# Performance work log

Hardware: AMD Instinct MI355X
Metric: run time of the kernel (lower is better)

The kernel has to match this reference:

```python
import jax, jax.numpy as jnp
import numpy as np

B, T, D_MODEL, N_HEADS = 2, 2048, 1024, 16
HEAD_DIM = D_MODEL // N_HEADS          # 64
CODE_SIZE = HEAD_DIM // 4              # 16


def setup_inputs() -> dict:
    key = jax.random.key(0)
    k1, k2, k3, k4 = jax.random.split(key, 4)
    x = jax.random.normal(k1, (B, T, D_MODEL), dtype=jnp.float32)
    # nn.Linear weights (out_features, in_features), fan-in init scale
    w_qkv = jax.random.normal(k2, (3 * D_MODEL, D_MODEL), dtype=jnp.float32) / np.sqrt(D_MODEL)
    w_out = jax.random.normal(k3, (D_MODEL, D_MODEL), dtype=jnp.float32) / np.sqrt(D_MODEL)
    fc_code = jax.random.normal(k4, (1, N_HEADS, CODE_SIZE, HEAD_DIM), dtype=jnp.float32)
    return {"x": x, "w_qkv": w_qkv, "w_out": w_out, "fc_code": fc_code}


def reference(x, w_qkv, w_out, fc_code):
    Bx, Tx, _ = x.shape
    scale = HEAD_DIM ** (-0.5)
    qkv = x @ w_qkv.T                                   # (B,T,3*d_model)
    # split_heads with Hs=head_dim on 3*d_model -> (B, 3*nH, T, Hs), then chunk on head axis
    qkv = qkv.reshape(Bx, Tx, 3 * N_HEADS, HEAD_DIM).transpose(0, 2, 1, 3)
    q, k, v = qkv[:, :N_HEADS], qkv[:, N_HEADS:2 * N_HEADS], qkv[:, 2 * N_HEADS:]
    code = fc_code[0]                                   # (nH, C, Hs)
    q = jnp.einsum('bhtd,hcd->bhtc', q, code) * scale   # (B,H,T,C)
    k = jnp.einsum('bhtd,hcd->bhtc', k, code) * scale
    q = jax.nn.softmax(q, axis=-1) * scale
    # causal branch (mask is None)
    k_exp = jnp.exp(k - jnp.max(k, axis=2, keepdims=True))       # (B,H,T,C)
    k_exp_cumsum = jnp.cumsum(k_exp, axis=2)                      # (B,H,T,C)
    kv_cumsum = jnp.cumsum(jnp.einsum('bhtc,bhtd->bhtcd', k_exp, v), axis=2)  # (B,H,T,C,D)
    kv = kv_cumsum / (k_exp_cumsum[..., None] + 1e-9)
    xo = jnp.einsum('bhtc,bhtcd->bhtd', q, kv)                    # (B,H,T,D)
    xo = xo.transpose(0, 2, 1, 3).reshape(Bx, Tx, D_MODEL)        # cat_heads
    return xo @ w_out.T
```

## Files before the change

### kernel.cpp

```cpp
#include <hip/hip_runtime.h>
#include <math.h>

#define B_    2
#define T_    2048
#define D_    1024
#define H_    16
#define HD_   64
#define C_    16
#define SCALE_ 0.125f
#define L_    128
#define NC_   16
#define QKP_  512

typedef __attribute__((ext_vector_type(8))) short short8;
typedef __attribute__((ext_vector_type(4))) float f32x4;

__device__ inline float b2f(uint32_t u16) {
    return __uint_as_float(u16 << 16);
}
__device__ inline ushort f2b(float f) {
    uint32_t u = __float_as_uint(f);
    return (ushort)((u + 0x7FFFu + ((u >> 16) & 1u)) >> 16);
}
__device__ inline uint32_t pack2(float a, float b) {
    return (uint32_t)f2b(a) | ((uint32_t)f2b(b) << 16);
}
__device__ inline void unpack2(uint32_t w, float& a, float& b) {
    a = b2f(w & 0xffffu); b = __uint_as_float(w & 0xffff0000u);
}
__device__ inline void unpack8(uint4 raw, float* dst) {
    unpack2(raw.x, dst[0], dst[1]);
    unpack2(raw.y, dst[2], dst[3]);
    unpack2(raw.z, dst[4], dst[5]);
    unpack2(raw.w, dst[6], dst[7]);
}
__device__ __forceinline__ void gll16(const ushort* g, ushort* l) {
    __builtin_amdgcn_global_load_lds(
        (const __attribute__((address_space(1))) void*)g,
        (__attribute__((address_space(3))) void*)l, 16, 0, 0);
}

__global__ __launch_bounds__(256)
void prep_inputs_kernel(const float* __restrict__ x, const float* __restrict__ w_qkv,
                        const float* __restrict__ w_out, const float* __restrict__ code,
                        ushort* __restrict__ xb, ushort* __restrict__ WallB,
                        ushort* __restrict__ WoB) {
    const int bid = blockIdx.x;
    if (bid < 3072) {
        const float* in;
        ushort* out;
        int i;
        if (bid < 2048) {
            in = x; out = xb;
            i = bid * 2048 + threadIdx.x * 8;
        } else {
            const int sub = bid - 2048;
            const int isW = sub >> 9;
            in = isW ? w_out : (w_qkv + (size_t)2048 * 1024);
            out = isW ? WoB : (WallB + (size_t)512 * 1024);
            i = (sub & 511) * 2048 + threadIdx.x * 8;
        }
        float4 a = *(const float4*)(in + i);
        float4 b = *(const float4*)(in + i + 4);
        uint4 o;
        o.x = pack2(a.x, a.y); o.y = pack2(a.z, a.w);
        o.z = pack2(b.x, b.y); o.w = pack2(b.z, b.w);
        *(uint4*)(out + i) = o;
    } else {
        const int sub = bid - 3072;
        const int isK = sub >> 8;
        const int row = sub & 255;
        const int h = row >> 4;
        __shared__ float cs[HD_];
        if (threadIdx.x < HD_) cs[threadIdx.x] = code[row * HD_ + threadIdx.x];
        __syncthreads();
        const float* wbase = w_qkv + (size_t)(isK * D_ + h * HD_) * D_;
        ushort* outp = WallB + (size_t)(isK * 256 + row) * D_;
        for (int e = threadIdx.x; e < D_; e += 256) {
            float acc = 0.f;
            #pragma unroll 8
            for (int d = 0; d < HD_; ++d) acc += wbase[(size_t)d * D_ + e] * cs[d];
            outp[e] = f2b(acc * SCALE_);
        }
    }
}

template<int MODE>
__global__ __launch_bounds__(256)
void gemm_bf16_kernel(const ushort* __restrict__ A, const ushort* __restrict__ Bw,
                      void* __restrict__ Cv, ushort* __restrict__ vTout,
                      int M, int N, int K) {
    __shared__ ushort As[2][128 * 64];
    __shared__ ushort Bs[2][64 * 64];
    const int tid  = threadIdx.x;
    const int wave = tid >> 6;
    const int lane = tid & 63;

    const int gx = gridDim.x;
    int f = blockIdx.y * gx + blockIdx.x;
    const int nwg = gx * gridDim.y;
    if ((nwg & 7) == 0) f = (f & 7) * (nwg >> 3) + (f >> 3);
    const int row0 = (f / gx) * 128;
    const int col0 = (f % gx) * 64;

    f32x4 acc[2][4];
    #pragma unroll
    for (int m = 0; m < 2; ++m)
        #pragma unroll
        for (int n = 0; n < 4; ++n) acc[m][n] = (f32x4){0.f, 0.f, 0.f, 0.f};

    const int srow = lane >> 3;
    const int kA   = ((lane & 7) ^ srow) << 3;
    const int lane15 = lane & 15;
    const int lhi    = lane >> 4;
    const int axor   = (lane15 & 7) << 4;

    const int NT = K >> 6;

    auto STAGE = [&](int buf, int kk) {
        #pragma unroll
        for (int i = 0; i < 6; ++i) {
            const int sg = wave * 6 + i;
            if (sg < 16) {
                const int r = sg * 8 + srow;
                gll16(A + (size_t)(row0 + r) * K + kk + kA, &As[buf][sg * 512]);
            } else {
                const int sb = sg - 16;
                const int r = sb * 8 + srow;
                gll16(Bw + (size_t)(col0 + r) * K + kk + kA, &Bs[buf][sb * 512]);
            }
        }
    };

    STAGE(0, 0);
    __syncthreads();

    for (int it = 0; it < NT; ++it) {
        const int cur = it & 1;
        if (it + 1 < NT) STAGE(cur ^ 1, (it + 1) << 6);
        const char* Ab = (const char*)As[cur];
        const char* Bb = (const char*)Bs[cur];
        #pragma unroll
        for (int s = 0; s < 2; ++s) {
            short8 af[2], bf[4];
            #pragma unroll
            for (int m = 0; m < 2; ++m) {
                const int r = wave * 32 + m * 16 + lane15;
                const int off = (r * 128 + s * 64 + lhi * 16) ^ axor;
                af[m] = *(const short8*)(Ab + off);
            }
            #pragma unroll
            for (int n = 0; n < 4; ++n) {
                const int r = n * 16 + lane15;
                const int off = (r * 128 + s * 64 + lhi * 16) ^ axor;
                bf[n] = *(const short8*)(Bb + off);
            }
            #pragma unroll
            for (int m = 0; m < 2; ++m)
                #pragma unroll
                for (int n = 0; n < 4; ++n)
                    acc[m][n] = __builtin_amdgcn_mfma_f32_16x16x32_bf16(
                        af[m], bf[n], acc[m][n], 0, 0, 0);
        }
        __syncthreads();
    }

    #pragma unroll
    for (int m = 0; m < 2; ++m) {
        #pragma unroll
        for (int n = 0; n < 4; ++n) {
            const int row = row0 + wave * 32 + m * 16 + lhi * 4;
            const int col = col0 + n * 16 + lane15;
            if (MODE == 0) {
                float* C = (float*)Cv;
                #pragma unroll
                for (int j = 0; j < 4; ++j)
                    C[(size_t)(row + j) * N + col] = acc[m][n][j];
            } else if (MODE == 1) {
                ushort* C = (ushort*)Cv;
                #pragma unroll
                for (int j = 0; j < 4; ++j)
                    C[(size_t)(row + j) * N + col] = f2b(acc[m][n][j]);
            } else {
                if (col0 < 512) {
                    ushort* C = (ushort*)Cv;
                    #pragma unroll
                    for (int j = 0; j < 4; ++j)
                        C[(size_t)(row + j) * QKP_ + col] = f2b(acc[m][n][j]);
                } else {
                    const int dg = col - 512;
                    const int h = dg >> 6, d = dg & 63;
                    const int b = row >> 11;
                    const int t = row & 2047;
                    ushort* p = vTout + ((size_t)((b * 16 + h) * 64 + d)) * 2048 + t;
                    *(uint2*)p = make_uint2(pack2(acc[m][n][0], acc[m][n][1]),
                                            pack2(acc[m][n][2], acc[m][n][3]));
                }
            }
        }
    }
}

__global__ __launch_bounds__(256)
void prep_attn_kernel(const ushort* __restrict__ qkcv, const ushort* __restrict__ vT,
                      float* __restrict__ ke_loc, float* __restrict__ kv_loc) {
    const int bid = blockIdx.x;
    const int chunk = bid & (NC_ - 1);
    const int bh = bid >> 4;
    const int b = bh >> 4, h = bh & 15;
    const int t0 = chunk * L_;
    const int tid = threadIdx.x;
    __shared__ float ke_s[L_][C_];
    __shared__ float gsum[C_][16];

    {
        const int t = tid >> 1, c0 = (tid & 1) * 8;
        uint4 raw = *(const uint4*)(qkcv + (size_t)(b * T_ + t0 + t) * QKP_ + 256 + h * C_ + c0);
        float f[8]; unpack8(raw, f);
        #pragma unroll
        for (int j = 0; j < 8; ++j) ke_s[t][c0 + j] = __expf(f[j]);
    }
    __syncthreads();

    const int d = tid & 63;
    const int cw = tid >> 6;
    const ushort* vrow = vT + ((size_t)(bh * 64 + d)) * 2048 + t0;
    float a0 = 0.f, a1 = 0.f, a2 = 0.f, a3 = 0.f;
    for (int kb = 0; kb < 16; ++kb) {
        uint4 raw = *(const uint4*)(vrow + kb * 8);
        float v8[8]; unpack8(raw, v8);
        #pragma unroll
        for (int u = 0; u < 8; ++u) {
            const int t = kb * 8 + u;
            a0 += ke_s[t][cw * 4 + 0] * v8[u];
            a1 += ke_s[t][cw * 4 + 1] * v8[u];
            a2 += ke_s[t][cw * 4 + 2] * v8[u];
            a3 += ke_s[t][cw * 4 + 3] * v8[u];
        }
    }
    float* kvb = kv_loc + (size_t)bid * 1024 + d;
    kvb[(cw * 4 + 0) * 64] = a0;
    kvb[(cw * 4 + 1) * 64] = a1;
    kvb[(cw * 4 + 2) * 64] = a2;
    kvb[(cw * 4 + 3) * 64] = a3;

    {
        const int cc = tid & 15, g = tid >> 4;
        float s = 0.f;
        #pragma unroll
        for (int u = 0; u < 8; ++u) s += ke_s[g * 8 + u][cc];
        gsum[cc][g] = s;
    }
    __syncthreads();
    if (tid < C_) {
        float s = 0.f;
        #pragma unroll
        for (int g = 0; g < 16; ++g) s += gsum[tid][g];
        ke_loc[(size_t)bid * C_ + tid] = s;
    }
}

__global__ __launch_bounds__(256)
void intra_kernel(const ushort* __restrict__ qkcv, const ushort* __restrict__ vT,
                  const float* __restrict__ ke_loc, const float* __restrict__ kv_loc,
                  ushort* __restrict__ xob) {
    const int bid = blockIdx.x;
    const int chunk = bid & (NC_ - 1);
    const int bh = bid >> 4;
    const int b = bh >> 4, h = bh & 15;
    const int t0 = chunk * L_;
    const int tid = threadIdx.x;
    const int wave = tid >> 6, lane = tid & 63;
    const int l15 = lane & 15, lhi = lane >> 4;

    __shared__ __align__(16) ushort ke_bf[128 * 32];
    __shared__ __align__(16) ushort qn_bf[128 * 32];
    __shared__ __align__(16) ushort Vt_s[64 * 128];
    __shared__ __align__(16) ushort Pl[128 * 128];
    __shared__ __align__(16) ushort S0t[64 * 32];
    __shared__ float kesum_s[128][16];
    __shared__ float gsum[16][16];
    __shared__ float e0s[16];

    char* keB = (char*)ke_bf;
    char* qnB = (char*)qn_bf;
    char* vtB = (char*)Vt_s;
    char* plB = (char*)Pl;
    char* s0B = (char*)S0t;

    {
        const int t = tid >> 1, c0 = (tid & 1) * 8;
        uint4 raw = *(const uint4*)(qkcv + (size_t)(b * T_ + t0 + t) * QKP_ + 256 + h * C_ + c0);
        float f[8]; unpack8(raw, f);
        uint4 o;
        o.x = pack2(__expf(f[0]), __expf(f[1]));
        o.y = pack2(__expf(f[2]), __expf(f[3]));
        o.z = pack2(__expf(f[4]), __expf(f[5]));
        o.w = pack2(__expf(f[6]), __expf(f[7]));
        const int swz = ((t >> 1) & 3) << 4;
        *(uint4*)(keB + ((t * 64 + c0 * 2) ^ swz)) = o;
        *(uint4*)(keB + ((t * 64 + 32 + c0 * 2) ^ swz)) = make_uint4(0, 0, 0, 0);
    }
    {
        const int d = tid >> 2, q = tid & 3;
        const ushort* src = vT + ((size_t)bh * 64 + d) * 2048 + t0 + q * 32;
        const int swz = (d & 15) << 4;
        #pragma unroll
        for (int i = 0; i < 4; ++i) {
            uint4 raw = *(const uint4*)(src + i * 8);
            *(uint4*)(vtB + ((d * 256 + q * 64 + i * 16) ^ swz)) = raw;
        }
    }
    {
        const int c = tid >> 4;
        const int d0 = (tid & 15) * 4;
        const float* base = kv_loc + (size_t)(bh * NC_) * 1024 + c * 64 + d0;
        float s0 = 0.f, s1 = 0.f, s2 = 0.f, s3 = 0.f;
        for (int ch = 0; ch < chunk; ++ch) {
            float4 t4 = *(const float4*)(base + ch * 1024);
            s0 += t4.x; s1 += t4.y; s2 += t4.z; s3 += t4.w;
        }
        const float sp[4] = {s0, s1, s2, s3};
        #pragma unroll
        for (int j = 0; j < 4; ++j) {
            const int d = d0 + j;
            const int swz2 = ((d >> 1) & 3) << 4;
            *(ushort*)(s0B + ((d * 64 + c * 2) ^ swz2)) = f2b(sp[j]);
        }
        const int dz = tid >> 2;
        const int off = 32 + (tid & 3) * 8;
        const int swzz = ((dz >> 1) & 3) << 4;
        *(uint2*)(s0B + ((dz * 64 + off) ^ swzz)) = make_uint2(0, 0);
    }
    if (tid < 16) {
        float s = 0.f;
        for (int ch = 0; ch < chunk; ++ch)
            s += ke_loc[(size_t)(bh * NC_ + ch) * C_ + tid];
        e0s[tid] = s;
    }
    __syncthreads();

    {
        const int cc = tid & 15, g = tid >> 4;
        float s = 0.f;
        #pragma unroll
        for (int u = 0; u < 8; ++u) {
            const int t = g * 8 + u;
            s += b2f(*(const ushort*)(keB + ((t * 64 + cc * 2) ^ (((t >> 1) & 3) << 4))));
        }
        gsum[cc][g] = s;
    }
    __syncthreads();
    if (tid < 16) {
        float run = e0s[tid];
        #pragma unroll
        for (int g = 0; g < 16; ++g) { float tmp = gsum[tid][g]; gsum[tid][g] = run; run += tmp; }
    }
    __syncthreads();
    {
        const int cc = tid & 15, g = tid >> 4;
        float run = gsum[cc][g];
        #pragma unroll
        for (int u = 0; u < 8; ++u) {
            const int t = g * 8 + u;
            run += b2f(*(const ushort*)(keB + ((t * 64 + cc * 2) ^ (((t >> 1) & 3) << 4))));
            kesum_s[t][cc] = run;
        }
    }
    __syncthreads();

    if (tid < 128) {
        const int t = tid;
        const ushort* qrow = qkcv + (size_t)(b * T_ + t0 + t) * QKP_ + h * C_;
        float qv[16];
        uint4 r0 = *(const uint4*)qrow, r1 = *(const uint4*)(qrow + 8);
        unpack8(r0, qv); unpack8(r1, qv + 8);
        float m = qv[0];
        #pragma unroll
        for (int c = 1; c < 16; ++c) m = fmaxf(m, qv[c]);
        float sum = 0.f;
        #pragma unroll
        for (int c = 0; c < 16; ++c) { qv[c] = __expf(qv[c] - m); sum += qv[c]; }
        const float inv = SCALE_ / sum;
        #pragma unroll
        for (int c = 0; c < 16; ++c) qv[c] = qv[c] * inv / (kesum_s[t][c] + 1e-9f);
        uint4 o0, o1;
        o0.x = pack2(qv[0], qv[1]);   o0.y = pack2(qv[2], qv[3]);
        o0.z = pack2(qv[4], qv[5]);   o0.w = pack2(qv[6], qv[7]);
        o1.x = pack2(qv[8], qv[9]);   o1.y = pack2(qv[10], qv[11]);
        o1.z = pack2(qv[12], qv[13]); o1.w = pack2(qv[14], qv[15]);
        const int swz = ((t >> 1) & 3) << 4;
        *(uint4*)(qnB + ((t * 64) ^ swz)) = o0;
        *(uint4*)(qnB + ((t * 64 + 16) ^ swz)) = o1;
        *(uint4*)(qnB + ((t * 64 + 32) ^ swz)) = make_uint4(0, 0, 0, 0);
        *(uint4*)(qnB + ((t * 64 + 48) ^ swz)) = make_uint4(0, 0, 0, 0);
    }
    __syncthreads();

    #pragma unroll
    for (int sr = 0; sr < 2; ++sr) {
        const int sb = wave * 2 + sr;
        const int s_row = sb * 16 + l15;
        short8 af = *(const short8*)(keB + ((s_row * 64 + lhi * 16) ^ (((s_row >> 1) & 3) << 4)));
        #pragma unroll
        for (int tb = 0; tb < 8; ++tb) {
            f32x4 p = (f32x4){0.f, 0.f, 0.f, 0.f};
            if (tb >= sb) {
                const int t_col = tb * 16 + l15;
                short8 bf = *(const short8*)(qnB + ((t_col * 64 + lhi * 16) ^ (((t_col >> 1) & 3) << 4)));
                p = __builtin_amdgcn_mfma_f32_16x16x32_bf16(af, bf, p, 0, 0, 0);
                if (tb == sb) {
                    #pragma unroll
                    for (int j = 0; j < 4; ++j)
                        p[j] = (lhi * 4 + j > l15) ? 0.f : p[j];
                }
            }
            const int t_g = tb * 16 + l15;
            const int sbase = sb * 16 + lhi * 4;
            const int swz = (t_g & 15) << 4;
            *(uint32_t*)(plB + ((t_g * 256 + sbase * 2) ^ swz)) = pack2(p[0], p[1]);
            *(uint32_t*)(plB + ((t_g * 256 + sbase * 2 + 4) ^ swz)) = pack2(p[2], p[3]);
        }
    }
    __syncthreads();

    f32x4 acc[2][4];
    #pragma unroll
    for (int tt = 0; tt < 2; ++tt)
        #pragma unroll
        for (int dt = 0; dt < 4; ++dt) acc[tt][dt] = (f32x4){0.f, 0.f, 0.f, 0.f};

    const int trow = wave * 32;
    #pragma unroll
    for (int tt = 0; tt < 2; ++tt) {
        const int t_g = trow + tt * 16 + l15;
        short8 aq = *(const short8*)(qnB + ((t_g * 64 + lhi * 16) ^ (((t_g >> 1) & 3) << 4)));
        #pragma unroll
        for (int dt = 0; dt < 4; ++dt) {
            const int d = dt * 16 + l15;
            short8 bs = *(const short8*)(s0B + ((d * 64 + lhi * 16) ^ (((d >> 1) & 3) << 4)));
            acc[tt][dt] = __builtin_amdgcn_mfma_f32_16x16x32_bf16(aq, bs, acc[tt][dt], 0, 0, 0);
        }
        const int pswz = (t_g & 15) << 4;
        #pragma unroll
        for (int kb = 0; kb < 4; ++kb) {
            short8 ap = *(const short8*)(plB + ((t_g * 256 + kb * 64 + lhi * 16) ^ pswz));
            #pragma unroll
            for (int dt = 0; dt < 4; ++dt) {
                const int d = dt * 16 + l15;
                short8 bv = *(const short8*)(vtB + ((d * 256 + kb * 64 + lhi * 16) ^ ((d & 15) << 4)));
                acc[tt][dt] = __builtin_amdgcn_mfma_f32_16x16x32_bf16(ap, bv, acc[tt][dt], 0, 0, 0);
            }
        }
    }

    #pragma unroll
    for (int tt = 0; tt < 2; ++tt) {
        const int tg0 = t0 + trow + tt * 16 + lhi * 4;
        #pragma unroll
        for (int dt = 0; dt < 4; ++dt) {
            const int d = dt * 16 + l15;
            ushort* orow = xob + (size_t)(b * T_ + tg0) * D_ + h * HD_ + d;
            #pragma unroll
            for (int j = 0; j < 4; ++j)
                orow[(size_t)j * D_] = f2b(acc[tt][dt][j]);
        }
    }
}

extern "C" void kernel_launch(void* const* d_in, const int* in_sizes, int n_in,
                              void* d_out, int out_size, void* d_ws, size_t ws_size,
                              hipStream_t stream) {
    const float* x     = (const float*)d_in[0];
    const float* w_qkv = (const float*)d_in[1];
    const float* w_out = (const float*)d_in[2];
    const float* code  = (const float*)d_in[3];
    float* out = (float*)d_out;

    ushort* xb    = (ushort*)d_ws;
    ushort* WallB = xb + (size_t)4096 * 1024;
    ushort* WoB   = WallB + (size_t)1536 * 1024;
    ushort* qkcv  = WoB + (size_t)1024 * 1024;
    ushort* xob   = qkcv + (size_t)4096 * 512;
    ushort* vT    = xob + (size_t)4096 * 1024;
    float*  ke_loc = (float*)(vT + (size_t)32 * 64 * 2048);
    float*  kv_loc = ke_loc + 512 * 16;

    prep_inputs_kernel<<<3584, 256, 0, stream>>>(x, w_qkv, w_out, code, xb, WallB, WoB);

    gemm_bf16_kernel<2><<<dim3(24, 32), 256, 0, stream>>>(xb, WallB, qkcv, vT, 4096, 1536, 1024);

    prep_attn_kernel<<<512, 256, 0, stream>>>(qkcv, vT, ke_loc, kv_loc);
    intra_kernel<<<512, 256, 0, stream>>>(qkcv, vT, ke_loc, kv_loc, xob);

    gemm_bf16_kernel<0><<<dim3(16, 32), 256, 0, stream>>>(xob, WoB, out, nullptr, 4096, 1024, 1024);
}
```

Baseline: 84.72 us.

## Reuse weight loads across code rows in fold prep; widen intra kernel to 8 waves

After: 79.74 us. 5.9% less time.

```diff
diff --git a/kernel.cpp b/kernel.cpp
--- a/kernel.cpp
+++ b/kernel.cpp
@@ -68,20 +68,38 @@
         *(uint4*)(out + i) = o;
     } else {
         const int sub = bid - 3072;
-        const int isK = sub >> 8;
-        const int row = sub & 255;
-        const int h = row >> 4;
-        __shared__ float cs[HD_];
-        if (threadIdx.x < HD_) cs[threadIdx.x] = code[row * HD_ + threadIdx.x];
+        const int isK = sub >> 6;
+        const int h   = (sub >> 2) & 15;
+        const int eq  = sub & 3;
+        const int e   = eq * 256 + threadIdx.x;
+        __shared__ __align__(16) float cs[C_][HD_];
+        {
+            float* csf = &cs[0][0];
+            *(float4*)(csf + threadIdx.x * 4) =
+                *(const float4*)(code + h * 1024 + threadIdx.x * 4);
+        }
         __syncthreads();
-        const float* wbase = w_qkv + (size_t)(isK * D_ + h * HD_) * D_;
-        ushort* outp = WallB + (size_t)(isK * 256 + row) * D_;
-        for (int e = threadIdx.x; e < D_; e += 256) {
-            float acc = 0.f;
-            #pragma unroll 8
-            for (int d = 0; d < HD_; ++d) acc += wbase[(size_t)d * D_ + e] * cs[d];
-            outp[e] = f2b(acc * SCALE_);
-        }
+        const float* wbase = w_qkv + ((size_t)(isK * D_ + h * HD_)) * D_ + e;
+        float acc[C_];
+        #pragma unroll
+        for (int c = 0; c < C_; ++c) acc[c] = 0.f;
+        #pragma unroll 4
+        for (int db = 0; db < 16; ++db) {
+            const float w0 = wbase[(size_t)(db * 4 + 0) * D_];
+            const float w1 = wbase[(size_t)(db * 4 + 1) * D_];
+            const float w2 = wbase[(size_t)(db * 4 + 2) * D_];
+            const float w3 = wbase[(size_t)(db * 4 + 3) * D_];
+            #pragma unroll
+            for (int c = 0; c < C_; ++c) {
+                float4 cv = *(const float4*)&cs[c][db * 4];
+                acc[c] += w0 * cv.x; acc[c] += w1 * cv.y;
+                acc[c] += w2 * cv.z; acc[c] += w3 * cv.w;
+            }
+        }
+        ushort* outp = WallB + (size_t)(isK * 256 + h * 16) * D_ + e;
+        #pragma unroll
+        for (int c = 0; c < C_; ++c)
+            outp[(size_t)c * D_] = f2b(acc[c] * SCALE_);
     }
 }
 
@@ -260,7 +278,7 @@
     }
 }
 
-__global__ __launch_bounds__(256)
+__global__ __launch_bounds__(512)
 void intra_kernel(const ushort* __restrict__ qkcv, const ushort* __restrict__ vT,
                   const float* __restrict__ ke_loc, const float* __restrict__ kv_loc,
                   ushort* __restrict__ xob) {
@@ -288,7 +306,7 @@
     char* plB = (char*)Pl;
     char* s0B = (char*)S0t;
 
-    {
+    if (tid < 256) {
         const int t = tid >> 1, c0 = (tid & 1) * 8;
         uint4 raw = *(const uint4*)(qkcv + (size_t)(b * T_ + t0 + t) * QKP_ + 256 + h * C_ + c0);
         float f[8]; unpack8(raw, f);
@@ -302,16 +320,16 @@
         *(uint4*)(keB + ((t * 64 + 32 + c0 * 2) ^ swz)) = make_uint4(0, 0, 0, 0);
     }
     {
-        const int d = tid >> 2, q = tid & 3;
-        const ushort* src = vT + ((size_t)bh * 64 + d) * 2048 + t0 + q * 32;
+        const int d = tid >> 3, qq = tid & 7;
+        const ushort* src = vT + ((size_t)bh * 64 + d) * 2048 + t0 + qq * 16;
         const int swz = (d & 15) << 4;
         #pragma unroll
-        for (int i = 0; i < 4; ++i) {
-            uint4 raw = *(const uint4*)(src + i * 8);
-            *(uint4*)(vtB + ((d * 256 + q * 64 + i * 16) ^ swz)) = raw;
-        }
-    }
-    {
+        for (int ii = 0; ii < 2; ++ii) {
+            uint4 raw = *(const uint4*)(src + ii * 8);
+            *(uint4*)(vtB + ((d * 256 + qq * 32 + ii * 16) ^ swz)) = raw;
+        }
+    }
+    if (tid < 256) {
         const int c = tid >> 4;
         const int d0 = (tid & 15) * 4;
         const float* base = kv_loc + (size_t)(bh * NC_) * 1024 + c * 64 + d0;
@@ -340,7 +358,7 @@
     }
     __syncthreads();
 
-    {
+    if (tid < 256) {
         const int cc = tid & 15, g = tid >> 4;
         float s = 0.f;
         #pragma unroll
@@ -357,7 +375,7 @@
         for (int g = 0; g < 16; ++g) { float tmp = gsum[tid][g]; gsum[tid][g] = run; run += tmp; }
     }
     __syncthreads();
-    {
+    if (tid < 256) {
         const int cc = tid & 15, g = tid >> 4;
         float run = gsum[cc][g];
         #pragma unroll
@@ -397,9 +415,8 @@
     }
     __syncthreads();
 
-    #pragma unroll
-    for (int sr = 0; sr < 2; ++sr) {
-        const int sb = wave * 2 + sr;
+    {
+        const int sb = wave;
         const int s_row = sb * 16 + l15;
         short8 af = *(const short8*)(keB + ((s_row * 64 + lhi * 16) ^ (((s_row >> 1) & 3) << 4)));
         #pragma unroll
@@ -424,22 +441,18 @@
     }
     __syncthreads();
 
-    f32x4 acc[2][4];
+    f32x4 acc4[4];
     #pragma unroll
-    for (int tt = 0; tt < 2; ++tt)
-        #pragma unroll
-        for (int dt = 0; dt < 4; ++dt) acc[tt][dt] = (f32x4){0.f, 0.f, 0.f, 0.f};
-
-    const int trow = wave * 32;
-    #pragma unroll
-    for (int tt = 0; tt < 2; ++tt) {
-        const int t_g = trow + tt * 16 + l15;
+    for (int dt = 0; dt < 4; ++dt) acc4[dt] = (f32x4){0.f, 0.f, 0.f, 0.f};
+
+    {
+        const int t_g = wave * 16 + l15;
         short8 aq = *(const short8*)(qnB + ((t_g * 64 + lhi * 16) ^ (((t_g >> 1) & 3) << 4)));
         #pragma unroll
         for (int dt = 0; dt < 4; ++dt) {
             const int d = dt * 16 + l15;
             short8 bs = *(const short8*)(s0B + ((d * 64 + lhi * 16) ^ (((d >> 1) & 3) << 4)));
-            acc[tt][dt] = __builtin_amdgcn_mfma_f32_16x16x32_bf16(aq, bs, acc[tt][dt], 0, 0, 0);
+            acc4[dt] = __builtin_amdgcn_mfma_f32_16x16x32_bf16(aq, bs, acc4[dt], 0, 0, 0);
         }
         const int pswz = (t_g & 15) << 4;
         #pragma unroll
@@ -449,21 +462,20 @@
             for (int dt = 0; dt < 4; ++dt) {
                 const int d = dt * 16 + l15;
                 short8 bv = *(const short8*)(vtB + ((d * 256 + kb * 64 + lhi * 16) ^ ((d & 15) << 4)));
-                acc[tt][dt] = __builtin_amdgcn_mfma_f32_16x16x32_bf16(ap, bv, acc[tt][dt], 0, 0, 0);
-            }
-        }
-    }
-
-    #pragma unroll
-    for (int tt = 0; tt < 2; ++tt) {
-        const int tg0 = t0 + trow + tt * 16 + lhi * 4;
+                acc4[dt] = __builtin_amdgcn_mfma_f32_16x16x32_bf16(ap, bv, acc4[dt], 0, 0, 0);
+            }
+        }
+    }
+
+    {
+        const int tg0 = t0 + wave * 16 + lhi * 4;
         #pragma unroll
         for (int dt = 0; dt < 4; ++dt) {
             const int d = dt * 16 + l15;
             ushort* orow = xob + (size_t)(b * T_ + tg0) * D_ + h * HD_ + d;
             #pragma unroll
             for (int j = 0; j < 4; ++j)
-                orow[(size_t)j * D_] = f2b(acc[tt][dt][j]);
+                orow[(size_t)j * D_] = f2b(acc4[dt][j]);
         }
     }
 }
@@ -486,12 +498,12 @@
     float*  ke_loc = (float*)(vT + (size_t)32 * 64 * 2048);
     float*  kv_loc = ke_loc + 512 * 16;
 
-    prep_inputs_kernel<<<3584, 256, 0, stream>>>(x, w_qkv, w_out, code, xb, WallB, WoB);
+    prep_inputs_kernel<<<3200, 256, 0, stream>>>(x, w_qkv, w_out, code, xb, WallB, WoB);
 
     gemm_bf16_kernel<2><<<dim3(24, 32), 256, 0, stream>>>(xb, WallB, qkcv, vT, 4096, 1536, 1024);
 
     prep_attn_kernel<<<512, 256, 0, stream>>>(qkcv, vT, ke_loc, kv_loc);
-    intra_kernel<<<512, 256, 0, stream>>>(qkcv, vT, ke_loc, kv_loc, xob);
+    intra_kernel<<<512, 512, 0, stream>>>(qkcv, vT, ke_loc, kv_loc, xob);
 
     gemm_bf16_kernel<0><<<dim3(16, 32), 256, 0, stream>>>(xob, WoB, out, nullptr, 4096, 1024, 1024);
 }
```
